# Performance work log

Hardware: AMD Instinct MI355X
Metric: run time of the kernel (lower is better)

## Reference

```python
import jax, jax.numpy as jnp
import numpy as np

D_MODEL = 1024
N_HEADS = 16
HEAD_DIM = D_MODEL // N_HEADS
ROPE_THETA = 10000.0


def _apply_rope(t, pos):
    # t: [B, H, S, hd]; pos: [B, S] int. Half-split (NeoX-style) rotation.
    hd = t.shape[-1]
    inv_freq = 1.0 / (ROPE_THETA ** (jnp.arange(0, hd, 2, dtype=t.dtype) / hd))  # [hd/2]
    ang = pos.astype(t.dtype)[:, None, :, None] * inv_freq  # [B, 1, S, hd/2]
    cos, sin = jnp.cos(ang), jnp.sin(ang)
    t1, t2 = t[..., 0::2], t[..., 1::2]
    r1 = t1 * cos - t2 * sin
    r2 = t1 * sin + t2 * cos
    # interleave back
    return jnp.stack([r1, r2], axis=-1).reshape(t.shape)


def setup_inputs() -> dict:
    key = jax.random.key(0)
    k1, k2, k3 = jax.random.split(key, 3)
    B, S = 4, 2048
    x = jax.random.normal(k1, (B, S, D_MODEL), dtype=jnp.float32)
    positions = jnp.broadcast_to(jnp.arange(S, dtype=jnp.int32), (B, S))
    Wqkv = jax.random.normal(k2, (3 * D_MODEL, D_MODEL), dtype=jnp.float32) * (1.0 / np.sqrt(D_MODEL))
    bqkv = jnp.zeros((3 * D_MODEL,), dtype=jnp.float32)
    Wo = jax.random.normal(k3, (D_MODEL, D_MODEL), dtype=jnp.float32) * (1.0 / np.sqrt(D_MODEL))
    bo = jnp.zeros((D_MODEL,), dtype=jnp.float32)
    return {"x": x, "positions": positions, "Wqkv": Wqkv, "bqkv": bqkv, "Wo": Wo, "bo": bo}


def reference(x, positions, Wqkv, bqkv, Wo, bo):
    B, S, D = x.shape
    # fused QKV projection (torch Linear: x @ W^T + b)
    qkv = x @ Wqkv.T + bqkv                      # [B, S, 3D]
    q, k, v = jnp.split(qkv, 3, axis=-1)
    def to_heads(t):
        return t.reshape(B, S, N_HEADS, HEAD_DIM).transpose(0, 2, 1, 3)  # [B, H, S, hd]
    q, k, v = to_heads(q), to_heads(k), to_heads(v)
    q = _apply_rope(q, positions)
    k = _apply_rope(k, positions)
    scale = 1.0 / np.sqrt(HEAD_DIM)
    scores = jnp.einsum('bhqd,bhkd->bhqk', q, k) * scale   # [B, H, S, S]
    causal = jnp.tril(jnp.ones((S, S), dtype=bool))
    scores = jnp.where(causal, scores, jnp.finfo(scores.dtype).min)
    attn = jax.nn.softmax(scores, axis=-1)
    h = jnp.einsum('bhqk,bhkd->bhqd', attn, v)             # [B, H, S, hd]
    h = h.transpose(0, 2, 1, 3).reshape(B, S, D)
    return h @ Wo.T + bo
```

## Files before the change

### kernel.cpp

```cpp
#include <hip/hip_runtime.h>

#define DEV static __device__ __forceinline__

typedef __attribute__((ext_vector_type(8))) short short8;
typedef __attribute__((ext_vector_type(4))) short short4v;
typedef __attribute__((ext_vector_type(4))) float f32x4;
typedef __attribute__((ext_vector_type(4))) unsigned short ushort4v;
typedef __attribute__((ext_vector_type(4))) float float4v;

#define DM 1024
#define NH 16
#define HD 64
#define SS 2048
#define TOK 8192

DEV unsigned short f2bf(float f) {
  union { float f; unsigned u; } v; v.f = f;
  unsigned r = v.u + 0x7FFFu + ((v.u >> 16) & 1u);
  return (unsigned short)(r >> 16);
}
DEV float bf2f(unsigned short h) {
  union { unsigned u; float f; } v; v.u = ((unsigned)h) << 16;
  return v.f;
}

#define MFMA16x32(a, b, c) __builtin_amdgcn_mfma_f32_16x16x32_bf16((a), (b), (c), 0, 0, 0)

DEV f32x4 mfma_pv(short4v a, short4v b, f32x4 c) {
#if __has_builtin(__builtin_amdgcn_mfma_f32_16x16x16bf16_1k)
  return __builtin_amdgcn_mfma_f32_16x16x16bf16_1k(a, b, c, 0, 0, 0);
#else
  f32x4 d;
  asm("v_mfma_f32_16x16x16_bf16 %0, %1, %2, %3" : "=&v"(d) : "v"(a), "v"(b), "v"(c));
  return d;
#endif
}

DEV void gload_lds16(const unsigned short* g, unsigned short* l) {
  __builtin_amdgcn_global_load_lds(
      (const __attribute__((address_space(1))) void*)g,
      (__attribute__((address_space(3))) void*)l, 16, 0, 0);
}

__global__ __launch_bounds__(256) void k_cvt(const float* __restrict__ in,
                                             unsigned short* __restrict__ out, int n4) {
  int i = blockIdx.x * 256 + threadIdx.x;
  if (i >= n4) return;
  float4v v = ((const float4v*)in)[i];
  ushort4v o;
  o[0] = f2bf(v[0]); o[1] = f2bf(v[1]); o[2] = f2bf(v[2]); o[3] = f2bf(v[3]);
  ((ushort4v*)out)[i] = o;
}

__global__ __launch_bounds__(256) void k_tab(const int* __restrict__ pos,
                                             float* __restrict__ tc, float* __restrict__ ts) {
  int i = blockIdx.x * 256 + threadIdx.x;
  int t = i >> 5, fi = i & 31;
  float p = (float)pos[t];
  float inv = powf(10000.0f, -(float)fi / 32.0f);
  float a = p * inv;
  float sv, cv;
  sincosf(a, &sv, &cv);
  tc[i] = cv;
  ts[i] = sv;
}

__global__ __launch_bounds__(256) void k_rope(unsigned short* __restrict__ Q,
                                              unsigned short* __restrict__ K,
                                              const float* __restrict__ tc,
                                              const float* __restrict__ ts) {
  int idx = blockIdx.x * 256 + threadIdx.x;
  int bh = idx >> 11, s = idx & 2047, b = bh >> 4;
  const float* tcp = tc + ((size_t)(b * SS + s)) * 32;
  const float* tsp = ts + ((size_t)(b * SS + s)) * 32;
  size_t base = (size_t)idx * 64;
  for (int which = 0; which < 2; ++which) {
    unsigned short* P = which ? K : Q;
    short8* rp = (short8*)(P + base);
#pragma unroll
    for (int ch = 0; ch < 8; ++ch) {
      short8 v = rp[ch];
      short8 r;
#pragma unroll
      for (int p = 0; p < 4; ++p) {
        int pi = ch * 4 + p;
        float e = bf2f((unsigned short)v[2 * p]);
        float o = bf2f((unsigned short)v[2 * p + 1]);
        float c = tcp[pi], sn = tsp[pi];
        r[2 * p]     = (short)f2bf(e * c - o * sn);
        r[2 * p + 1] = (short)f2bf(e * sn + o * c);
      }
      rp[ch] = r;
    }
  }
}

template <int MODE>
__global__ __launch_bounds__(512) void k_gemm3(
    const unsigned short* __restrict__ A, const unsigned short* __restrict__ Bm,
    const float* __restrict__ bias, void* __restrict__ out0, void* __restrict__ out1,
    void* __restrict__ out2, int M, int N, int K) {
  __shared__ __align__(16) unsigned short Abuf[3][256 * 64];
  __shared__ __align__(16) unsigned short Bbuf[3][128 * 64];
  const int tid = threadIdx.x;
  const int wid = tid >> 6, lane = tid & 63;
  const int l16 = lane & 15, lq = lane >> 4;
  const int wr = wid >> 1, wc = wid & 1;
  const int m0 = blockIdx.y * 256, n0 = blockIdx.x * 128;
  const int r8 = lane >> 3, c8 = lane & 7;
  const int NT = K >> 6;
  const int sx = l16 & 7;

#define STAGE_G3(T, BSEL)                                                           \
  {                                                                                 \
    int k0_ = (T) << 6;                                                             \
    unsigned short* ab_ = Abuf[BSEL];                                               \
    unsigned short* bb_ = Bbuf[BSEL];                                               \
    _Pragma("unroll")                                                               \
    for (int i_ = 0; i_ < 4; ++i_) {                                                \
      int o_ = wid * 4 + i_;                                                        \
      gload_lds16(A + (size_t)(m0 + o_ * 8 + r8) * K + k0_ + ((c8 ^ r8) << 3),      \
                  &ab_[o_ * 512]);                                                  \
    }                                                                               \
    _Pragma("unroll")                                                               \
    for (int i_ = 0; i_ < 2; ++i_) {                                                \
      int o_ = wid * 2 + i_;                                                        \
      gload_lds16(Bm + (size_t)(n0 + o_ * 8 + r8) * K + k0_ + ((c8 ^ r8) << 3),     \
                  &bb_[o_ * 512]);                                                  \
    }                                                                               \
  }

  f32x4 acc[4][4];
#pragma unroll
  for (int i = 0; i < 4; i++)
#pragma unroll
    for (int j = 0; j < 4; j++) acc[i][j] = (f32x4){0.f, 0.f, 0.f, 0.f};

  STAGE_G3(0, 0)
  STAGE_G3(1, 1)
  asm volatile("s_waitcnt vmcnt(6)" ::: "memory");
  __builtin_amdgcn_s_barrier();
  __builtin_amdgcn_sched_barrier(0);

  int cb = 0, sb = 2;
  for (int t = 0; t < NT; ++t) {
    if (t + 2 < NT) STAGE_G3(t + 2, sb)
    const unsigned short* Ab = Abuf[cb];
    const unsigned short* Bb = Bbuf[cb];
#pragma unroll
    for (int kk = 0; kk < 2; ++kk) {
      int sw0 = ((kk * 4 + lq) ^ sx) << 3;
      short8 af[4], bfr[4];
#pragma unroll
      for (int mi = 0; mi < 4; ++mi)
        af[mi] = *(const short8*)&Ab[(wr * 64 + mi * 16 + l16) * 64 + sw0];
#pragma unroll
      for (int ni = 0; ni < 4; ++ni)
        bfr[ni] = *(const short8*)&Bb[(wc * 64 + ni * 16 + l16) * 64 + sw0];
#pragma unroll
      for (int mi = 0; mi < 4; ++mi)
#pragma unroll
        for (int ni = 0; ni < 4; ++ni)
          acc[mi][ni] = MFMA16x32(af[mi], bfr[ni], acc[mi][ni]);
    }
    if (t + 1 < NT) {
      if (t + 3 <= NT) {
        asm volatile("s_waitcnt vmcnt(6)" ::: "memory");
      } else {
        asm volatile("s_waitcnt vmcnt(0)" ::: "memory");
      }
      __builtin_amdgcn_s_barrier();
      __builtin_amdgcn_sched_barrier(0);
    }
    cb = (cb == 2) ? 0 : cb + 1;
    sb = (sb == 2) ? 0 : sb + 1;
  }
#undef STAGE_G3

  if (MODE == 0) {
    float* C = (float*)out0;
#pragma unroll
    for (int mi = 0; mi < 4; ++mi) {
      int row = m0 + wr * 64 + mi * 16 + lq * 4;
#pragma unroll
      for (int ni = 0; ni < 4; ++ni) {
        int col = n0 + wc * 64 + ni * 16 + l16;
        float bv = bias[col];
#pragma unroll
        for (int j = 0; j < 4; ++j)
          C[(size_t)(row + j) * N + col] = acc[mi][ni][j] + bv;
      }
    }
  } else {
    unsigned short* Qb = (unsigned short*)out0;
    unsigned short* Kb = (unsigned short*)out1;
    unsigned short* Vt = (unsigned short*)out2;
#pragma unroll
    for (int mi = 0; mi < 4; ++mi) {
      int row = m0 + wr * 64 + mi * 16 + lq * 4;
      int b = row >> 11, s = row & 2047;
#pragma unroll
      for (int ni = 0; ni < 4; ++ni) {
        int col = n0 + wc * 64 + ni * 16 + l16;
        int sel = col >> 10;
        int hh = (col >> 6) & 15;
        int d = col & 63;
        float bv = bias[col];
        if (sel < 2) {
          unsigned short* P = sel ? Kb : Qb;
          size_t p = ((size_t)(b * NH + hh) * SS + s) * 64 + d;
#pragma unroll
          for (int j = 0; j < 4; ++j)
            P[p + (size_t)j * 64] = f2bf(acc[mi][ni][j] + bv);
        } else {
          size_t p = ((size_t)(b * NH + hh) * 64 + d) * SS + s;
          ushort4v o;
#pragma unroll
          for (int j = 0; j < 4; ++j) o[j] = f2bf(acc[mi][ni][j] + bv);
          *(ushort4v*)&Vt[p] = o;
        }
      }
    }
  }
}

__global__ __launch_bounds__(256) void k_attn(const unsigned short* __restrict__ Q,
                                              const unsigned short* __restrict__ K,
                                              const unsigned short* __restrict__ Vt,
                                              unsigned short* __restrict__ H) {
  __shared__ __align__(16) unsigned short Kbuf[2 * 4096];
  __shared__ __align__(16) unsigned short Vbuf[2 * 4096];

  int lin = blockIdx.x;
  int bh = lin & 63;
  int p = lin >> 6;
  int b = bh >> 4, h = bh & 15;
  int wid = threadIdx.x >> 6, lane = threadIdx.x & 63;
  int l16 = lane & 15, lq = lane >> 4;
  int sx = l16 & 7;
  const unsigned short* Qh = Q + (size_t)bh * SS * 64;
  const unsigned short* Kh = K + (size_t)bh * SS * 64;
  const unsigned short* Vh = Vt + (size_t)bh * 64 * SS;

  for (int seg = 0; seg < 2; ++seg) {
    int g = seg ? (31 - p) : p;
    int qbase = g * 64 + wid * 16;
    int qrow = qbase + l16;
    int ntk = g + 1;

    short8 aq[2];
    {
      const unsigned short* qp = Qh + (size_t)qrow * 64 + lq * 8;
      aq[0] = *(const short8*)qp;
      aq[1] = *(const short8*)(qp + 32);
    }
    f32x4 o[4];
#pragma unroll
    for (int i = 0; i < 4; ++i) o[i] = (f32x4){0.f, 0.f, 0.f, 0.f};
    float lsum = 0.f;

#pragma unroll
    for (int i = 0; i < 2; ++i) {
      int c = threadIdx.x + (i << 8);
      int row = c >> 3, col = ((c & 7) ^ (row & 7)) << 3;
      gload_lds16(Kh + (size_t)row * 64 + col, &Kbuf[c * 8]);
      gload_lds16(Vh + (size_t)row * SS + col, &Vbuf[c * 8]);
    }
    __syncthreads();

    int cur = 0;
    for (int kt = 0; kt < ntk; ++kt) {
      if (kt + 1 < ntk) {
        int kb1 = (kt + 1) << 6;
        int nb_ = (cur ^ 1) * 4096;
#pragma unroll
        for (int i = 0; i < 2; ++i) {
          int c = threadIdx.x + (i << 8);
          int row = c >> 3, col = ((c & 7) ^ (row & 7)) << 3;
          gload_lds16(Kh + (size_t)(kb1 + row) * 64 + col, &Kbuf[nb_ + c * 8]);
          gload_lds16(Vh + (size_t)row * SS + kb1 + col, &Vbuf[nb_ + c * 8]);
        }
      }
      int kb = kt << 6;
      const unsigned short* Kb_ = &Kbuf[cur * 4096];
      const unsigned short* Vb_ = &Vbuf[cur * 4096];

      f32x4 sacc[4];
#pragma unroll
      for (int nb = 0; nb < 4; ++nb) {
        int r = nb * 16 + l16;
        short8 bk0 = *(const short8*)&Kb_[r * 64 + ((lq ^ sx) << 3)];
        short8 bk1 = *(const short8*)&Kb_[r * 64 + (((4 | lq) ^ sx) << 3)];
        f32x4 z = (f32x4){0.f, 0.f, 0.f, 0.f};
        z = MFMA16x32(bk0, aq[0], z);
        z = MFMA16x32(bk1, aq[1], z);
        sacc[nb] = z;
      }
      float sc[4][4];
#pragma unroll
      for (int nb = 0; nb < 4; ++nb)
#pragma unroll
        for (int j = 0; j < 4; ++j) sc[nb][j] = sacc[nb][j] * 0.18033688f;
      if (kt == g) {
#pragma unroll
        for (int nb = 0; nb < 4; ++nb)
#pragma unroll
          for (int j = 0; j < 4; ++j) {
            int key = kb + nb * 16 + lq * 4 + j;
            if (key > qrow) sc[nb][j] = -1e30f;
          }
      }
      short4v pa[4];
#pragma unroll
      for (int nb = 0; nb < 4; ++nb) {
        float pv[4];
#pragma unroll
        for (int j = 0; j < 4; ++j) {
          float e;
          asm("v_exp_f32 %0, %1" : "=v"(e) : "v"(sc[nb][j]));
          lsum += e;
          pv[j] = e;
        }
        union { unsigned u[2]; short4v s4; } pk;
        asm("v_cvt_pk_bf16_f32 %0, %1, %2" : "=v"(pk.u[0]) : "v"(pv[0]), "v"(pv[1]));
        asm("v_cvt_pk_bf16_f32 %0, %1, %2" : "=v"(pk.u[1]) : "v"(pv[2]), "v"(pv[3]));
        pa[nb] = pk.s4;
      }
#pragma unroll
      for (int ni = 0; ni < 4; ++ni) {
        int row = ni * 16 + l16;
        f32x4 acc = o[ni];
#pragma unroll
        for (int nb = 0; nb < 4; ++nb) {
          int ch = (2 * nb + (lq >> 1)) ^ sx;
          short4v bv = *(const short4v*)&Vb_[row * 64 + ch * 8 + ((lq & 1) << 2)];
          acc = mfma_pv(pa[nb], bv, acc);
        }
        o[ni] = acc;
      }
      __syncthreads();
      cur ^= 1;
    }

    float red = lsum;
    red += __shfl_xor(red, 16, 64);
    red += __shfl_xor(red, 32, 64);
    float inv[4];
#pragma unroll
    for (int j = 0; j < 4; ++j) {
      int src = (lane & 48) + ((lane >> 4) & 3) * 4 + j;
      inv[j] = 1.0f / __shfl(red, src, 64);
    }
#pragma unroll
    for (int ni = 0; ni < 4; ++ni) {
      int d = h * 64 + ni * 16 + l16;
#pragma unroll
      for (int j = 0; j < 4; ++j) {
        int s = qbase + lq * 4 + j;
        H[((size_t)(b * SS + s)) * 1024 + d] = f2bf(o[ni][j] * inv[j]);
      }
    }
  }
}

extern "C" void kernel_launch(void* const* d_in, const int* in_sizes, int n_in,
                              void* d_out, int out_size, void* d_ws, size_t ws_size,
                              hipStream_t stream) {
  const float* x    = (const float*)d_in[0];
  const int*   pos  = (const int*)d_in[1];
  const float* Wqkv = (const float*)d_in[2];
  const float* bqkv = (const float*)d_in[3];
  const float* Wo   = (const float*)d_in[4];
  const float* bo   = (const float*)d_in[5];
  float* out = (float*)d_out;

  char* w = (char*)d_ws;
  unsigned short* x_bf    = (unsigned short*)(w + 0);
  unsigned short* h_bf    = x_bf;
  unsigned short* wqkv_bf = (unsigned short*)(w + 16777216);
  unsigned short* wo_bf   = (unsigned short*)(w + 23068672);
  unsigned short* Qb      = (unsigned short*)(w + 25165824);
  unsigned short* Kb      = (unsigned short*)(w + 41943040);
  unsigned short* Vt      = (unsigned short*)(w + 58720256);
  float* tabc             = (float*)(w + 75497472);
  float* tabs             = (float*)(w + 76546048);

  k_cvt<<<8192, 256, 0, stream>>>(x, x_bf, 2097152);
  k_cvt<<<3072, 256, 0, stream>>>(Wqkv, wqkv_bf, 786432);
  k_cvt<<<1024, 256, 0, stream>>>(Wo, wo_bf, 262144);
  k_tab<<<1024, 256, 0, stream>>>(pos, tabc, tabs);
  k_gemm3<1><<<dim3(24, 32), 512, 0, stream>>>(x_bf, wqkv_bf, bqkv, Qb, Kb, Vt, TOK, 3072, DM);
  k_rope<<<512, 256, 0, stream>>>(Qb, Kb, tabc, tabs);
  k_attn<<<1024, 256, 0, stream>>>(Qb, Kb, Vt, h_bf);
  k_gemm3<0><<<dim3(8, 32), 512, 0, stream>>>(h_bf, wo_bf, bo, out, nullptr, nullptr, TOK, DM, DM);
}
```

Measured before the change: 214.9 us.

## Rework GEMM to 4 waves with 128x64 per-wave tiles, fragment-ordered LDS, XCD block remap

Replaces the 8-wave 256x128 GEMM with a 4-wave version at the same block tile: each wave now computes 128x64 with 8x4 MFMA accumulators, and the K step shrinks to 32. Shared memory is laid out directly in MFMA fragment order rather than XOR-swizzled rows, and a 1D grid is remapped so consecutive virtual tiles land on the same XCD for better L2 reuse. Launch bounds request two blocks per CU. The larger per-wave tile raises register pressure and the smaller K step doubles barrier count per GEMM.

```diff
diff --git a/kernel.cpp b/kernel.cpp
--- a/kernel.cpp
+++ b/kernel.cpp
@@ -96,75 +96,78 @@
 }
 
 template <int MODE>
-__global__ __launch_bounds__(512) void k_gemm3(
+__global__ __launch_bounds__(256, 2) void k_gemm4(
     const unsigned short* __restrict__ A, const unsigned short* __restrict__ Bm,
     const float* __restrict__ bias, void* __restrict__ out0, void* __restrict__ out1,
     void* __restrict__ out2, int M, int N, int K) {
-  __shared__ __align__(16) unsigned short Abuf[3][256 * 64];
-  __shared__ __align__(16) unsigned short Bbuf[3][128 * 64];
+  __shared__ __align__(16) unsigned short Abuf[3][8192];
+  __shared__ __align__(16) unsigned short Bbuf[3][4096];
   const int tid = threadIdx.x;
   const int wid = tid >> 6, lane = tid & 63;
   const int l16 = lane & 15, lq = lane >> 4;
-  const int wr = wid >> 1, wc = wid & 1;
-  const int m0 = blockIdx.y * 256, n0 = blockIdx.x * 128;
-  const int r8 = lane >> 3, c8 = lane & 7;
-  const int NT = K >> 6;
-  const int sx = l16 & 7;
-
-#define STAGE_G3(T, BSEL)                                                           \
-  {                                                                                 \
-    int k0_ = (T) << 6;                                                             \
-    unsigned short* ab_ = Abuf[BSEL];                                               \
-    unsigned short* bb_ = Bbuf[BSEL];                                               \
-    _Pragma("unroll")                                                               \
-    for (int i_ = 0; i_ < 4; ++i_) {                                                \
-      int o_ = wid * 4 + i_;                                                        \
-      gload_lds16(A + (size_t)(m0 + o_ * 8 + r8) * K + k0_ + ((c8 ^ r8) << 3),      \
-                  &ab_[o_ * 512]);                                                  \
-    }                                                                               \
-    _Pragma("unroll")                                                               \
-    for (int i_ = 0; i_ < 2; ++i_) {                                                \
-      int o_ = wid * 2 + i_;                                                        \
-      gload_lds16(Bm + (size_t)(n0 + o_ * 8 + r8) * K + k0_ + ((c8 ^ r8) << 3),     \
-                  &bb_[o_ * 512]);                                                  \
-    }                                                                               \
-  }
-
-  f32x4 acc[4][4];
-#pragma unroll
-  for (int i = 0; i < 4; i++)
+  const int wm = wid >> 1, wn = wid & 1;
+  const int NT = K >> 5;
+
+  int gx = N >> 7;
+  int nwg = gx * (M >> 8);
+  int chunk = nwg >> 3;
+  int bid = blockIdx.x;
+  int virt = (bid & 7) * chunk + (bid >> 3);
+  int m0 = (virt / gx) << 8;
+  int n0 = (virt % gx) << 7;
+
+#define STAGE_G4(T, BSEL)                                                          \
+  {                                                                                \
+    int k0_ = (T) << 5;                                                            \
+    unsigned short* ab_ = Abuf[BSEL];                                              \
+    unsigned short* bb_ = Bbuf[BSEL];                                              \
+    _Pragma("unroll")                                                              \
+    for (int i_ = 0; i_ < 4; ++i_) {                                               \
+      int cell = tid + (i_ << 8);                                                  \
+      int l_ = cell & 15, ko_ = (cell >> 4) & 3, mf_ = cell >> 6;                  \
+      gload_lds16(A + (size_t)(m0 + mf_ * 16 + l_) * K + k0_ + ko_ * 8,            \
+                  &ab_[cell * 8]);                                                 \
+    }                                                                              \
+    _Pragma("unroll")                                                              \
+    for (int i_ = 0; i_ < 2; ++i_) {                                               \
+      int cell = tid + (i_ << 8);                                                  \
+      int l_ = cell & 15, ko_ = (cell >> 4) & 3, mf_ = cell >> 6;                  \
+      gload_lds16(Bm + (size_t)(n0 + mf_ * 16 + l_) * K + k0_ + ko_ * 8,           \
+                  &bb_[cell * 8]);                                                 \
+    }                                                                              \
+  }
+
+  f32x4 acc[8][4];
+#pragma unroll
+  for (int i = 0; i < 8; i++)
 #pragma unroll
     for (int j = 0; j < 4; j++) acc[i][j] = (f32x4){0.f, 0.f, 0.f, 0.f};
 
-  STAGE_G3(0, 0)
-  STAGE_G3(1, 1)
+  STAGE_G4(0, 0)
+  STAGE_G4(1, 1)
   asm volatile("s_waitcnt vmcnt(6)" ::: "memory");
   __builtin_amdgcn_s_barrier();
   __builtin_amdgcn_sched_barrier(0);
 
   int cb = 0, sb = 2;
   for (int t = 0; t < NT; ++t) {
-    if (t + 2 < NT) STAGE_G3(t + 2, sb)
+    if (t + 2 < NT) STAGE_G4(t + 2, sb)
     const unsigned short* Ab = Abuf[cb];
     const unsigned short* Bb = Bbuf[cb];
-#pragma unroll
-    for (int kk = 0; kk < 2; ++kk) {
-      int sw0 = ((kk * 4 + lq) ^ sx) << 3;
-      short8 af[4], bfr[4];
-#pragma unroll
-      for (int mi = 0; mi < 4; ++mi)
-        af[mi] = *(const short8*)&Ab[(wr * 64 + mi * 16 + l16) * 64 + sw0];
+    short8 af[8], bfr[4];
+#pragma unroll
+    for (int mi = 0; mi < 8; ++mi)
+      af[mi] = *(const short8*)&Ab[(((wm * 8 + mi) * 4 + lq) * 16 + l16) * 8];
+#pragma unroll
+    for (int ni = 0; ni < 4; ++ni)
+      bfr[ni] = *(const short8*)&Bb[(((wn * 4 + ni) * 4 + lq) * 16 + l16) * 8];
+#pragma unroll
+    for (int mi = 0; mi < 8; ++mi)
 #pragma unroll
       for (int ni = 0; ni < 4; ++ni)
-        bfr[ni] = *(const short8*)&Bb[(wc * 64 + ni * 16 + l16) * 64 + sw0];
-#pragma unroll
-      for (int mi = 0; mi < 4; ++mi)
-#pragma unroll
-        for (int ni = 0; ni < 4; ++ni)
-          acc[mi][ni] = MFMA16x32(af[mi], bfr[ni], acc[mi][ni]);
-    }
+        acc[mi][ni] = MFMA16x32(af[mi], bfr[ni], acc[mi][ni]);
     if (t + 1 < NT) {
-      if (t + 3 <= NT) {
+      if (t + 2 < NT) {
         asm volatile("s_waitcnt vmcnt(6)" ::: "memory");
       } else {
         asm volatile("s_waitcnt vmcnt(0)" ::: "memory");
@@ -175,16 +178,16 @@
     cb = (cb == 2) ? 0 : cb + 1;
     sb = (sb == 2) ? 0 : sb + 1;
   }
-#undef STAGE_G3
+#undef STAGE_G4
 
   if (MODE == 0) {
     float* C = (float*)out0;
 #pragma unroll
-    for (int mi = 0; mi < 4; ++mi) {
-      int row = m0 + wr * 64 + mi * 16 + lq * 4;
+    for (int mi = 0; mi < 8; ++mi) {
+      int row = m0 + (wm * 8 + mi) * 16 + lq * 4;
 #pragma unroll
       for (int ni = 0; ni < 4; ++ni) {
-        int col = n0 + wc * 64 + ni * 16 + l16;
+        int col = n0 + (wn * 4 + ni) * 16 + l16;
         float bv = bias[col];
 #pragma unroll
         for (int j = 0; j < 4; ++j)
@@ -196,12 +199,12 @@
     unsigned short* Kb = (unsigned short*)out1;
     unsigned short* Vt = (unsigned short*)out2;
 #pragma unroll
-    for (int mi = 0; mi < 4; ++mi) {
-      int row = m0 + wr * 64 + mi * 16 + lq * 4;
+    for (int mi = 0; mi < 8; ++mi) {
+      int row = m0 + (wm * 8 + mi) * 16 + lq * 4;
       int b = row >> 11, s = row & 2047;
 #pragma unroll
       for (int ni = 0; ni < 4; ++ni) {
-        int col = n0 + wc * 64 + ni * 16 + l16;
+        int col = n0 + (wn * 4 + ni) * 16 + l16;
         int sel = col >> 10;
         int hh = (col >> 6) & 15;
         int d = col & 63;
@@ -389,8 +392,8 @@
   k_cvt<<<3072, 256, 0, stream>>>(Wqkv, wqkv_bf, 786432);
   k_cvt<<<1024, 256, 0, stream>>>(Wo, wo_bf, 262144);
   k_tab<<<1024, 256, 0, stream>>>(pos, tabc, tabs);
-  k_gemm3<1><<<dim3(24, 32), 512, 0, stream>>>(x_bf, wqkv_bf, bqkv, Qb, Kb, Vt, TOK, 3072, DM);
+  k_gemm4<1><<<768, 256, 0, stream>>>(x_bf, wqkv_bf, bqkv, Qb, Kb, Vt, TOK, 3072, DM);
   k_rope<<<512, 256, 0, stream>>>(Qb, Kb, tabc, tabs);
   k_attn<<<1024, 256, 0, stream>>>(Qb, Kb, Vt, h_bf);
-  k_gemm3<0><<<dim3(8, 32), 512, 0, stream>>>(h_bf, wo_bf, bo, out, nullptr, nullptr, TOK, DM, DM);
-}
+  k_gemm4<0><<<256, 256, 0, stream>>>(h_bf, wo_bf, bo, out, nullptr, nullptr, TOK, DM, DM);
+}
```

Result: slower. 260.2 us (+21.1%).

## Fuse RoPE into QKV GEMM epilogue and remap workgroups for XCD locality

Applied to the files above, without the earlier changes.

Removes the separate RoPE kernel by applying the rotation in the QKV GEMM epilogue, using a lane shuffle to fetch the paired even/odd element and reading the cos/sin tables per row. This avoids a full extra read and write pass over Q and K. It also switches to a 1D grid with a block-id remap that gives each of the 8 XCDs a contiguous chunk of tiles, aiming for better L2 reuse. The epilogue gains table loads and shuffles in exchange.

```diff
diff --git a/kernel.cpp b/kernel.cpp
--- a/kernel.cpp
+++ b/kernel.cpp
@@ -65,51 +65,29 @@
   ts[i] = sv;
 }
 
-__global__ __launch_bounds__(256) void k_rope(unsigned short* __restrict__ Q,
-                                              unsigned short* __restrict__ K,
-                                              const float* __restrict__ tc,
-                                              const float* __restrict__ ts) {
-  int idx = blockIdx.x * 256 + threadIdx.x;
-  int bh = idx >> 11, s = idx & 2047, b = bh >> 4;
-  const float* tcp = tc + ((size_t)(b * SS + s)) * 32;
-  const float* tsp = ts + ((size_t)(b * SS + s)) * 32;
-  size_t base = (size_t)idx * 64;
-  for (int which = 0; which < 2; ++which) {
-    unsigned short* P = which ? K : Q;
-    short8* rp = (short8*)(P + base);
-#pragma unroll
-    for (int ch = 0; ch < 8; ++ch) {
-      short8 v = rp[ch];
-      short8 r;
-#pragma unroll
-      for (int p = 0; p < 4; ++p) {
-        int pi = ch * 4 + p;
-        float e = bf2f((unsigned short)v[2 * p]);
-        float o = bf2f((unsigned short)v[2 * p + 1]);
-        float c = tcp[pi], sn = tsp[pi];
-        r[2 * p]     = (short)f2bf(e * c - o * sn);
-        r[2 * p + 1] = (short)f2bf(e * sn + o * c);
-      }
-      rp[ch] = r;
-    }
-  }
-}
-
 template <int MODE>
 __global__ __launch_bounds__(512) void k_gemm3(
     const unsigned short* __restrict__ A, const unsigned short* __restrict__ Bm,
     const float* __restrict__ bias, void* __restrict__ out0, void* __restrict__ out1,
-    void* __restrict__ out2, int M, int N, int K) {
+    void* __restrict__ out2, const float* __restrict__ tabc,
+    const float* __restrict__ tabs, int M, int N, int K) {
   __shared__ __align__(16) unsigned short Abuf[3][256 * 64];
   __shared__ __align__(16) unsigned short Bbuf[3][128 * 64];
   const int tid = threadIdx.x;
   const int wid = tid >> 6, lane = tid & 63;
   const int l16 = lane & 15, lq = lane >> 4;
   const int wr = wid >> 1, wc = wid & 1;
-  const int m0 = blockIdx.y * 256, n0 = blockIdx.x * 128;
   const int r8 = lane >> 3, c8 = lane & 7;
   const int NT = K >> 6;
   const int sx = l16 & 7;
+
+  const int MT = M >> 8;
+  const int nwg = (N >> 7) * MT;
+  const int chunk = nwg >> 3;
+  const int bid = blockIdx.x;
+  const int virt = (bid & 7) * chunk + (bid >> 3);
+  const int m0 = (virt % MT) << 8;
+  const int n0 = (virt / MT) << 7;
 
 #define STAGE_G3(T, BSEL)                                                           \
   {                                                                                 \
@@ -118,15 +96,15 @@
     unsigned short* bb_ = Bbuf[BSEL];                                               \
     _Pragma("unroll")                                                               \
     for (int i_ = 0; i_ < 4; ++i_) {                                                \
-      int o_ = wid * 4 + i_;                                                        \
-      gload_lds16(A + (size_t)(m0 + o_ * 8 + r8) * K + k0_ + ((c8 ^ r8) << 3),      \
-                  &ab_[o_ * 512]);                                                  \
+      int c_ = wid * 4 + i_;                                                        \
+      gload_lds16(A + (size_t)(m0 + c_ * 8 + r8) * K + k0_ + ((c8 ^ r8) << 3),      \
+                  &ab_[c_ * 512]);                                                  \
     }                                                                               \
     _Pragma("unroll")                                                               \
     for (int i_ = 0; i_ < 2; ++i_) {                                                \
-      int o_ = wid * 2 + i_;                                                        \
-      gload_lds16(Bm + (size_t)(n0 + o_ * 8 + r8) * K + k0_ + ((c8 ^ r8) << 3),     \
-                  &bb_[o_ * 512]);                                                  \
+      int c_ = wid * 2 + i_;                                                        \
+      gload_lds16(Bm + (size_t)(n0 + c_ * 8 + r8) * K + k0_ + ((c8 ^ r8) << 3),     \
+                  &bb_[c_ * 512]);                                                  \
     }                                                                               \
   }
 
@@ -195,25 +173,35 @@
     unsigned short* Qb = (unsigned short*)out0;
     unsigned short* Kb = (unsigned short*)out1;
     unsigned short* Vt = (unsigned short*)out2;
+    int sel0 = n0 >> 10;
 #pragma unroll
     for (int mi = 0; mi < 4; ++mi) {
       int row = m0 + wr * 64 + mi * 16 + lq * 4;
       int b = row >> 11, s = row & 2047;
+      (void)b; (void)s;
 #pragma unroll
       for (int ni = 0; ni < 4; ++ni) {
         int col = n0 + wc * 64 + ni * 16 + l16;
-        int sel = col >> 10;
         int hh = (col >> 6) & 15;
         int d = col & 63;
         float bv = bias[col];
-        if (sel < 2) {
-          unsigned short* P = sel ? Kb : Qb;
-          size_t p = ((size_t)(b * NH + hh) * SS + s) * 64 + d;
-#pragma unroll
-          for (int j = 0; j < 4; ++j)
-            P[p + (size_t)j * 64] = f2bf(acc[mi][ni][j] + bv);
+        if (sel0 < 2) {
+          unsigned short* P = sel0 ? Kb : Qb;
+          int pfr = d >> 1;
+          size_t p = ((size_t)((row >> 11) * NH + hh) * SS + (row & 2047)) * 64 + d;
+#pragma unroll
+          for (int j = 0; j < 4; ++j) {
+            float val = acc[mi][ni][j] + bv;
+            float part = __shfl_xor(val, 1, 64);
+            int rr = row + j;
+            float cv = tabc[((size_t)rr << 5) + pfr];
+            float sv = tabs[((size_t)rr << 5) + pfr];
+            float outv = (d & 1) ? (part * sv + val * cv)
+                                 : (val * cv - part * sv);
+            P[p + (size_t)j * 64] = f2bf(outv);
+          }
         } else {
-          size_t p = ((size_t)(b * NH + hh) * 64 + d) * SS + s;
+          size_t p = ((size_t)((row >> 11) * NH + hh) * 64 + d) * SS + (row & 2047);
           ushort4v o;
 #pragma unroll
           for (int j = 0; j < 4; ++j) o[j] = f2bf(acc[mi][ni][j] + bv);
@@ -389,8 +377,7 @@
   k_cvt<<<3072, 256, 0, stream>>>(Wqkv, wqkv_bf, 786432);
   k_cvt<<<1024, 256, 0, stream>>>(Wo, wo_bf, 262144);
   k_tab<<<1024, 256, 0, stream>>>(pos, tabc, tabs);
-  k_gemm3<1><<<dim3(24, 32), 512, 0, stream>>>(x_bf, wqkv_bf, bqkv, Qb, Kb, Vt, TOK, 3072, DM);
-  k_rope<<<512, 256, 0, stream>>>(Qb, Kb, tabc, tabs);
+  k_gemm3<1><<<768, 512, 0, stream>>>(x_bf, wqkv_bf, bqkv, Qb, Kb, Vt, tabc, tabs, TOK, 3072, DM);
   k_attn<<<1024, 256, 0, stream>>>(Qb, Kb, Vt, h_bf);
-  k_gemm3<0><<<dim3(8, 32), 512, 0, stream>>>(h_bf, wo_bf, bo, out, nullptr, nullptr, TOK, DM, DM);
-}
+  k_gemm3<0><<<256, 512, 0, stream>>>(h_bf, wo_bf, bo, out, nullptr, nullptr, tabc, tabs, TOK, DM, DM);
+}
```

After: 208.5 us. 1.03x faster.
